# Performance work log

Measured on AMD Instinct MI355X. Metric: run time of the kernel, lower is better.

## Reference

```python
import jax, jax.numpy as jnp
import numpy as np


def _conv1d(x, w, b, pad):
    # x: (B, Cin, L), w: (Cout, Cin, K) -> (B, Cout, L)
    y = jax.lax.conv_general_dilated(x, w, window_strides=(1,), padding=[(pad, pad)],
                                     dimension_numbers=('NCH', 'OIH', 'NCH'))
    return y + b[None, :, None]


def setup_inputs() -> dict:
    V, E, H, D, K = 4096, 128, 256, 64, 512  # vocab, embed, hidden, code_dim, num_codes
    B, L = 16, 2048
    key = jax.random.key(0)
    ks = jax.random.split(key, 17)

    def g(k, shape, fan_in):
        return (jax.random.normal(k, shape, jnp.float32) / np.sqrt(fan_in)).astype(jnp.float32)

    x = jax.random.randint(ks[0], (B, L), 0, V)
    token_emb = (jax.random.normal(ks[1], (V, E), jnp.float32) * 0.02).at[0].set(0.0)  # pad_id=0
    # encoder convs: k3, k3, k1
    ew1 = g(ks[2], (H, E, 3), E * 3); eb1 = jnp.zeros((H,), jnp.float32)
    ew2 = g(ks[3], (H, H, 3), H * 3); eb2 = jnp.zeros((H,), jnp.float32)
    ew3 = g(ks[4], (D, H, 1), H);     eb3 = jnp.zeros((D,), jnp.float32)
    # VQ codebook: uniform(-1/K, 1/K)
    codebook = jax.random.uniform(ks[5], (K, D), jnp.float32, minval=-1.0 / K, maxval=1.0 / K)
    # decoder convs: k1, k3, k1
    dw1 = g(ks[6], (H, D, 1), D);     db1 = jnp.zeros((H,), jnp.float32)
    dw2 = g(ks[7], (H, H, 3), H * 3); db2 = jnp.zeros((H,), jnp.float32)
    dw3 = g(ks[8], (E, H, 1), H);     db3 = jnp.zeros((E,), jnp.float32)
    out_w = g(ks[9], (V, E), E);      out_b = jnp.zeros((V,), jnp.float32)
    return {"x": x, "token_emb": token_emb,
            "ew1": ew1, "eb1": eb1, "ew2": ew2, "eb2": eb2, "ew3": ew3, "eb3": eb3,
            "codebook": codebook,
            "dw1": dw1, "db1": db1, "dw2": dw2, "db2": db2, "dw3": dw3, "db3": db3,
            "out_w": out_w, "out_b": out_b}


def reference(x, token_emb, ew1, eb1, ew2, eb2, ew3, eb3, codebook,
              dw1, db1, dw2, db2, dw3, db3, out_w, out_b):
    B, L = x.shape
    emb = token_emb[x]                              # (B, L, E)
    h = jnp.transpose(emb, (0, 2, 1))               # (B, E, L)
    h = jax.nn.relu(_conv1d(h, ew1, eb1, 1))
    h = jax.nn.relu(_conv1d(h, ew2, eb2, 1))
    h = _conv1d(h, ew3, eb3, 0)
    z_e = jnp.transpose(h, (0, 2, 1))               # (B, L, D)
    D = z_e.shape[-1]
    # --- Vector quantization (eval mode: no EMA update) ---
    flat = z_e.reshape(-1, D)                       # (B*L, D)
    dists = (flat ** 2).sum(1, keepdims=True) - 2.0 * flat @ codebook.T + (codebook ** 2).sum(1)[None, :]
    codes = jnp.argmin(dists, axis=1)               # (B*L,)
    z_q = codebook[codes].reshape(B, L, D)
    z_q_st = z_e + jax.lax.stop_gradient(z_q - z_e)
    commit = jnp.mean((jax.lax.stop_gradient(z_e) - z_q) ** 2)
    loss_vq = 0.1 * commit                          # VQVAE passes commitment_cost=0.1
    # --- Decoder ---
    hd = jnp.transpose(z_q_st, (0, 2, 1))           # (B, D, L)
    hd = jax.nn.relu(_conv1d(hd, dw1, db1, 0))
    hd = jax.nn.relu(_conv1d(hd, dw2, db2, 1))
    hd = jax.nn.relu(_conv1d(hd, dw3, db3, 0))
    hd = jnp.transpose(hd, (0, 2, 1))               # (B, L, E)
    logits = hd @ out_w.T + out_b                   # (B, L, V)
    return logits, loss_vq, codes.reshape(B, L)
```

## Files before the change

### kernel.cpp

```cpp
#include <hip/hip_runtime.h>

constexpr int Bb = 16, Ll = 2048, Ee = 128, Hh = 256, Dd = 64, Kc = 512, Vv = 4096;
constexpr int NN = Bb * Ll;
constexpr int LOGITS = NN * Vv;

__global__ void transpose_w(const float* __restrict__ w, float* __restrict__ wt,
                            int Cout, int Cin, int KW) {
    int i = blockIdx.x * 256 + threadIdx.x;
    int total = Cout * Cin * KW;
    if (i >= total) return;
    int co  = i / (Cin * KW);
    int rem = i - co * (Cin * KW);
    int ci  = rem / KW;
    int k   = rem - ci * KW;
    wt[((size_t)(k * Cin + ci)) * Cout + co] = w[i];
}

__global__ void embed_kernel(const int* __restrict__ x,
                             const float4* __restrict__ te,
                             float4* __restrict__ out) {
    int gid = blockIdx.x * 256 + threadIdx.x;
    int n = gid >> 5;
    int c = gid & 31;
    out[gid] = te[((size_t)x[n] << 5) + c];
}

template <int KW, bool RELU, int BM, int BN, int TM, int TN>
__global__ __launch_bounds__(256) void gemm_conv(
    const float* __restrict__ A, const float* __restrict__ Wt,
    const float* __restrict__ bias, float* __restrict__ Y, int Cin, int Cout) {
    constexpr int BK = 16;
    const int tid = threadIdx.x;
    const int tx = tid % (BN / TN);
    const int ty = tid / (BN / TN);
    const int n0  = blockIdx.x * BM;
    const int co0 = blockIdx.y * BN;

    __shared__ float As[BK][BM + 4];
    __shared__ float Bs[BK][BN];

    float acc[TM][TN];
#pragma unroll
    for (int i = 0; i < TM; i++)
#pragma unroll
        for (int j = 0; j < TN; j++) acc[i][j] = 0.f;

    constexpr int A4 = BM * BK / (256 * 4);
    constexpr int B4 = BN * BK / (256 * 4);

    for (int k = 0; k < KW; ++k) {
        const int shift = k - (KW - 1) / 2;
        for (int ci0 = 0; ci0 < Cin; ci0 += BK) {
#pragma unroll
            for (int v = 0; v < A4; ++v) {
                int f4 = v * 256 + tid;
                int r  = f4 / (BK / 4);
                int c4 = f4 % (BK / 4);
                int n = n0 + r;
                float4 val = make_float4(0.f, 0.f, 0.f, 0.f);
                if (KW == 1) {
                    val = *(const float4*)(A + (size_t)n * Cin + ci0 + c4 * 4);
                } else {
                    int l  = n & (Ll - 1);
                    int sl = l + shift;
                    if ((unsigned)sl < (unsigned)Ll)
                        val = *(const float4*)(A + (size_t)(n + shift) * Cin + ci0 + c4 * 4);
                }
                As[c4 * 4 + 0][r] = val.x;
                As[c4 * 4 + 1][r] = val.y;
                As[c4 * 4 + 2][r] = val.z;
                As[c4 * 4 + 3][r] = val.w;
            }
#pragma unroll
            for (int v = 0; v < B4; ++v) {
                int f4 = v * 256 + tid;
                int c  = f4 / (BN / 4);
                int j4 = f4 % (BN / 4);
                float4 w4 = *(const float4*)(Wt + (size_t)(k * Cin + ci0 + c) * Cout + co0 + j4 * 4);
                *(float4*)(&Bs[c][j4 * 4]) = w4;
            }
            __syncthreads();
#pragma unroll
            for (int cc = 0; cc < BK; ++cc) {
                float a[TM], b[TN];
#pragma unroll
                for (int i = 0; i < TM; i += 4)
                    *(float4*)(&a[i]) = *(const float4*)(&As[cc][ty * TM + i]);
#pragma unroll
                for (int j = 0; j < TN; j += 4)
                    *(float4*)(&b[j]) = *(const float4*)(&Bs[cc][tx * TN + j]);
#pragma unroll
                for (int i = 0; i < TM; i++)
#pragma unroll
                    for (int j = 0; j < TN; j++)
                        acc[i][j] = fmaf(a[i], b[j], acc[i][j]);
            }
            __syncthreads();
        }
    }
#pragma unroll
    for (int i = 0; i < TM; i++) {
        int n = n0 + ty * TM + i;
#pragma unroll
        for (int j = 0; j < TN; j += 4) {
            int co = co0 + tx * TN + j;
            float4 r;
            r.x = acc[i][j + 0] + bias[co + 0];
            r.y = acc[i][j + 1] + bias[co + 1];
            r.z = acc[i][j + 2] + bias[co + 2];
            r.w = acc[i][j + 3] + bias[co + 3];
            if (RELU) {
                r.x = fmaxf(r.x, 0.f); r.y = fmaxf(r.y, 0.f);
                r.z = fmaxf(r.z, 0.f); r.w = fmaxf(r.w, 0.f);
            }
            *(float4*)(Y + (size_t)n * Cout + co) = r;
        }
    }
}

__global__ __launch_bounds__(256) void vq_kernel(
    const float* __restrict__ ze, const float* __restrict__ cb,
    int* __restrict__ codes_i, float* __restrict__ codes_f) {
    const int tid = threadIdx.x;
    const int tx = tid & 15, ty = tid >> 4;
    const int n0 = blockIdx.x * 64;

    __shared__ float Zs[Dd][64 + 4];
    __shared__ float Cs[Dd][64 + 4];
    __shared__ float bD[64][17];
    __shared__ int   bI[64][17];

#pragma unroll
    for (int v = 0; v < 4; ++v) {
        int f4 = v * 256 + tid;
        int row = f4 >> 4, d4 = f4 & 15;
        float4 z = *(const float4*)(ze + (size_t)(n0 + row) * Dd + d4 * 4);
        Zs[d4 * 4 + 0][row] = z.x;
        Zs[d4 * 4 + 1][row] = z.y;
        Zs[d4 * 4 + 2][row] = z.z;
        Zs[d4 * 4 + 3][row] = z.w;
    }

    float best[4];
    int   bidx[4];
#pragma unroll
    for (int i = 0; i < 4; i++) { best[i] = 3.4e38f; bidx[i] = 0; }

    for (int ch = 0; ch < Kc / 64; ++ch) {
        int c0 = ch * 64;
        __syncthreads();
#pragma unroll
        for (int v = 0; v < 4; ++v) {
            int f4 = v * 256 + tid;
            int j = f4 >> 4, d4 = f4 & 15;
            float4 w = *(const float4*)(cb + (size_t)(c0 + j) * Dd + d4 * 4);
            Cs[d4 * 4 + 0][j] = w.x;
            Cs[d4 * 4 + 1][j] = w.y;
            Cs[d4 * 4 + 2][j] = w.z;
            Cs[d4 * 4 + 3][j] = w.w;
        }
        __syncthreads();

        float dist[4][4];
#pragma unroll
        for (int i = 0; i < 4; i++)
#pragma unroll
            for (int j = 0; j < 4; j++) dist[i][j] = 0.f;

#pragma unroll 8
        for (int d = 0; d < Dd; ++d) {
            float a[4], b[4];
            *(float4*)a = *(const float4*)(&Zs[d][ty * 4]);
            *(float4*)b = *(const float4*)(&Cs[d][tx * 4]);
#pragma unroll
            for (int i = 0; i < 4; i++)
#pragma unroll
                for (int j = 0; j < 4; j++) {
                    float df = a[i] - b[j];
                    dist[i][j] = fmaf(df, df, dist[i][j]);
                }
        }
#pragma unroll
        for (int i = 0; i < 4; i++)
#pragma unroll
            for (int j = 0; j < 4; j++) {
                int ci = c0 + tx * 4 + j;
                if (dist[i][j] < best[i]) { best[i] = dist[i][j]; bidx[i] = ci; }
            }
    }
    __syncthreads();
#pragma unroll
    for (int i = 0; i < 4; i++) {
        bD[ty * 4 + i][tx] = best[i];
        bI[ty * 4 + i][tx] = bidx[i];
    }
    __syncthreads();
    if (tid < 64) {
        float bd = bD[tid][0];
        int   bi = bI[tid][0];
        for (int t = 1; t < 16; ++t) {
            float d = bD[tid][t];
            int   ix = bI[tid][t];
            if (d < bd || (d == bd && ix < bi)) { bd = d; bi = ix; }
        }
        codes_i[n0 + tid] = bi;
        codes_f[n0 + tid] = (float)bi;
    }
}

__global__ void gather_zq(const int* __restrict__ codes,
                          const float4* __restrict__ cb, float4* __restrict__ zq) {
    int gid = blockIdx.x * 256 + threadIdx.x;
    int n = gid >> 4, c = gid & 15;
    zq[gid] = cb[((size_t)codes[n] << 4) + c];
}

__global__ __launch_bounds__(256) void commit_partial(
    const float* __restrict__ ze, const float* __restrict__ zq,
    float* __restrict__ partial) {
    float s = 0.f;
    for (int i = blockIdx.x * 256 + threadIdx.x; i < NN * Dd; i += 1024 * 256) {
        float d = ze[i] - zq[i];
        s = fmaf(d, d, s);
    }
    for (int off = 32; off; off >>= 1) s += __shfl_down(s, off, 64);
    __shared__ float w[4];
    int lane = threadIdx.x & 63, wv = threadIdx.x >> 6;
    if (lane == 0) w[wv] = s;
    __syncthreads();
    if (threadIdx.x == 0) partial[blockIdx.x] = w[0] + w[1] + w[2] + w[3];
}

__global__ void commit_final(const float* __restrict__ partial, float* __restrict__ loss) {
    float s = 0.f;
    for (int i = threadIdx.x; i < 1024; i += 256) s += partial[i];
    for (int off = 32; off; off >>= 1) s += __shfl_down(s, off, 64);
    __shared__ float w[4];
    int lane = threadIdx.x & 63, wv = threadIdx.x >> 6;
    if (lane == 0) w[wv] = s;
    __syncthreads();
    if (threadIdx.x == 0)
        loss[0] = 0.1f * (w[0] + w[1] + w[2] + w[3]) / (float)(NN * Dd);
}

extern "C" void kernel_launch(void* const* d_in, const int* in_sizes, int n_in,
                              void* d_out, int out_size, void* d_ws, size_t ws_size,
                              hipStream_t stream) {
    const int*   x    = (const int*)d_in[0];
    const float* te   = (const float*)d_in[1];
    const float* ew1  = (const float*)d_in[2];
    const float* eb1  = (const float*)d_in[3];
    const float* ew2  = (const float*)d_in[4];
    const float* eb2  = (const float*)d_in[5];
    const float* ew3  = (const float*)d_in[6];
    const float* eb3  = (const float*)d_in[7];
    const float* cb   = (const float*)d_in[8];
    const float* dw1  = (const float*)d_in[9];
    const float* db1  = (const float*)d_in[10];
    const float* dw2  = (const float*)d_in[11];
    const float* db2  = (const float*)d_in[12];
    const float* dw3  = (const float*)d_in[13];
    const float* db3  = (const float*)d_in[14];
    const float* outw = (const float*)d_in[15];
    const float* outb = (const float*)d_in[16];

    char* ws = (char*)d_ws;
    size_t off = 0;
    auto alloc = [&](size_t bytes) -> void* {
        void* p = ws + off;
        off = (off + bytes + 255) & ~(size_t)255;
        return p;
    };
    float* bufA   = (float*)alloc((size_t)NN * Ee * 4);
    float* bufB   = (float*)alloc((size_t)NN * Hh * 4);
    float* bufC   = (float*)alloc((size_t)NN * Hh * 4);
    float* bufZ   = (float*)alloc((size_t)NN * Dd * 4);
    float* bufQ   = (float*)alloc((size_t)NN * Dd * 4);
    int*   codesi = (int*)alloc((size_t)NN * 4);
    float* part   = (float*)alloc(1024 * 4);
    float* wt_e1  = (float*)alloc((size_t)3 * Ee * Hh * 4);
    float* wt_e2  = (float*)alloc((size_t)3 * Hh * Hh * 4);
    float* wt_e3  = (float*)alloc((size_t)Hh * Dd * 4);
    float* wt_d1  = (float*)alloc((size_t)Dd * Hh * 4);
    float* wt_d2  = (float*)alloc((size_t)3 * Hh * Hh * 4);
    float* wt_d3  = (float*)alloc((size_t)Hh * Ee * 4);
    float* wt_o   = (float*)alloc((size_t)Ee * Vv * 4);

    float* out       = (float*)d_out;
    float* out_loss  = out + (size_t)LOGITS;
    float* out_codes = out_loss + 1;

    auto tg = [](int n) { return dim3((n + 255) / 256); };
    transpose_w<<<tg(Hh * Ee * 3), 256, 0, stream>>>(ew1, wt_e1, Hh, Ee, 3);
    transpose_w<<<tg(Hh * Hh * 3), 256, 0, stream>>>(ew2, wt_e2, Hh, Hh, 3);
    transpose_w<<<tg(Dd * Hh),     256, 0, stream>>>(ew3, wt_e3, Dd, Hh, 1);
    transpose_w<<<tg(Hh * Dd),     256, 0, stream>>>(dw1, wt_d1, Hh, Dd, 1);
    transpose_w<<<tg(Hh * Hh * 3), 256, 0, stream>>>(dw2, wt_d2, Hh, Hh, 3);
    transpose_w<<<tg(Ee * Hh),     256, 0, stream>>>(dw3, wt_d3, Ee, Hh, 1);
    transpose_w<<<tg(Vv * Ee),     256, 0, stream>>>(outw, wt_o, Vv, Ee, 1);

    embed_kernel<<<dim3(NN * 32 / 256), 256, 0, stream>>>(x, (const float4*)te, (float4*)bufA);

    gemm_conv<3, true, 128, 128, 8, 8><<<dim3(NN / 128, Hh / 128), 256, 0, stream>>>(bufA, wt_e1, eb1, bufB, Ee, Hh);
    gemm_conv<3, true, 128, 128, 8, 8><<<dim3(NN / 128, Hh / 128), 256, 0, stream>>>(bufB, wt_e2, eb2, bufC, Hh, Hh);
    gemm_conv<1, false, 64, 64, 4, 4><<<dim3(NN / 64, 1), 256, 0, stream>>>(bufC, wt_e3, eb3, bufZ, Hh, Dd);

    vq_kernel<<<dim3(NN / 64), 256, 0, stream>>>(bufZ, cb, codesi, out_codes);
    gather_zq<<<dim3(NN * 16 / 256), 256, 0, stream>>>(codesi, (const float4*)cb, (float4*)bufQ);
    commit_partial<<<dim3(1024), 256, 0, stream>>>(bufZ, bufQ, part);
    commit_final<<<dim3(1), 256, 0, stream>>>(part, out_loss);

    gemm_conv<1, true, 128, 128, 8, 8><<<dim3(NN / 128, Hh / 128), 256, 0, stream>>>(bufQ, wt_d1, db1, bufB, Dd, Hh);
    gemm_conv<3, true, 128, 128, 8, 8><<<dim3(NN / 128, Hh / 128), 256, 0, stream>>>(bufB, wt_d2, db2, bufC, Hh, Hh);
    gemm_conv<1, true, 128, 128, 8, 8><<<dim3(NN / 128, Ee / 128), 256, 0, stream>>>(bufC, wt_d3, db3, bufA, Hh, Ee);

    gemm_conv<1, false, 128, 128, 8, 8><<<dim3(NN / 128, Vv / 128), 256, 0, stream>>>(bufA, wt_o, outb, out, Ee, Vv);
}
```

Measured before the change: 1.413 ms.

## Compute output projection with bf16x3 split MFMA GEMM

Replaces the FP32 SIMT GEMM for the final vocab projection with a bf16 MFMA kernel. Each FP32 operand is split into hi and lo bf16 parts and laid out along an extended K dimension of 3*E, so one MFMA GEMM accumulates hi*hi + hi*lo + lo*hi and approximates FP32 accuracy. Operand tiles are loaded with direct global-to-LDS loads. This adds an activation split pass plus extra bf16 buffers, and its accuracy is below true FP32 because the lo*lo term is dropped.

```diff
diff --git a/kernel.cpp b/kernel.cpp
--- a/kernel.cpp
+++ b/kernel.cpp
@@ -3,6 +3,9 @@
 constexpr int Bb = 16, Ll = 2048, Ee = 128, Hh = 256, Dd = 64, Kc = 512, Vv = 4096;
 constexpr int NN = Bb * Ll;
 constexpr int LOGITS = NN * Vv;
+
+typedef __attribute__((ext_vector_type(8))) short bf16x8;
+typedef __attribute__((ext_vector_type(4))) float f32x4;
 
 __global__ void transpose_w(const float* __restrict__ w, float* __restrict__ wt,
                             int Cout, int Cin, int KW) {
@@ -23,6 +26,117 @@
     int n = gid >> 5;
     int c = gid & 31;
     out[gid] = te[((size_t)x[n] << 5) + c];
+}
+
+__device__ __forceinline__ unsigned short f2bf_rne(float f) {
+    unsigned int u = __float_as_uint(f);
+    unsigned int r = (u + 0x7fffu + ((u >> 16) & 1u)) >> 16;
+    return (unsigned short)r;
+}
+__device__ __forceinline__ float bf2f(unsigned short h) {
+    return __uint_as_float((unsigned int)h << 16);
+}
+
+template <bool LO_MID>
+__global__ void split3(const float* __restrict__ in, short* __restrict__ out, int K) {
+    int idx = blockIdx.x * 256 + threadIdx.x;
+    int m = idx / K;
+    int k = idx - m * K;
+    float a = in[idx];
+    unsigned short hi = f2bf_rne(a);
+    unsigned short lo = f2bf_rne(a - bf2f(hi));
+    size_t base = (size_t)m * (3 * K) + k;
+    out[base]         = (short)hi;
+    out[base + K]     = (short)(LO_MID ? lo : hi);
+    out[base + 2 * K] = (short)(LO_MID ? hi : lo);
+}
+
+__device__ __forceinline__ void gload16(const void* g, void* l) {
+    __builtin_amdgcn_global_load_lds(
+        (const __attribute__((address_space(1))) unsigned int*)g,
+        (__attribute__((address_space(3))) unsigned int*)l, 16, 0, 0);
+}
+
+template <bool RELU>
+__global__ __launch_bounds__(256) void gemm_mfma(
+    const short* __restrict__ A3, const short* __restrict__ B3,
+    const float* __restrict__ bias, float* __restrict__ Y,
+    int KK, int Nout) {
+    __shared__ short As[4096];
+    __shared__ short Bs[4096];
+
+    const int tid  = threadIdx.x;
+    const int lane = tid & 63;
+    const int wid  = tid >> 6;
+    const int ntile = Nout >> 7;
+    const int tm = blockIdx.x / ntile;
+    const int tn = blockIdx.x - tm * ntile;
+    const int m0 = tm << 7;
+    const int n0 = tn << 7;
+
+    const int wm = wid >> 1, wn = wid & 1;
+    const int lr = lane & 15;
+    const int kg = lane >> 4;
+
+    f32x4 acc[4][4];
+#pragma unroll
+    for (int i = 0; i < 4; ++i)
+#pragma unroll
+        for (int j = 0; j < 4; ++j)
+#pragma unroll
+            for (int q = 0; q < 4; ++q) acc[i][j][q] = 0.f;
+
+    const short* Ag = A3 + (size_t)m0 * KK;
+    const short* Bg = B3 + (size_t)n0 * KK;
+
+    for (int k0 = 0; k0 < KK; k0 += 32) {
+#pragma unroll
+        for (int j = 0; j < 2; ++j) {
+            const short* g = Ag + (size_t)(j * 64 + lane) * KK + k0 + wid * 8;
+            short* l = As + (size_t)(wid * 128 + j * 64) * 8;
+            gload16(g, l);
+        }
+#pragma unroll
+        for (int j = 0; j < 2; ++j) {
+            const short* g = Bg + (size_t)(j * 64 + lane) * KK + k0 + wid * 8;
+            short* l = Bs + (size_t)(wid * 128 + j * 64) * 8;
+            gload16(g, l);
+        }
+        __syncthreads();
+
+        bf16x8 af[4], bfr[4];
+#pragma unroll
+        for (int i = 0; i < 4; ++i)
+            af[i] = *reinterpret_cast<const bf16x8*>(
+                &As[(size_t)(kg * 128 + wm * 64 + i * 16 + lr) * 8]);
+#pragma unroll
+        for (int j = 0; j < 4; ++j)
+            bfr[j] = *reinterpret_cast<const bf16x8*>(
+                &Bs[(size_t)(kg * 128 + wn * 64 + j * 16 + lr) * 8]);
+#pragma unroll
+        for (int i = 0; i < 4; ++i)
+#pragma unroll
+            for (int j = 0; j < 4; ++j)
+                acc[i][j] = __builtin_amdgcn_mfma_f32_16x16x32_bf16(
+                    af[i], bfr[j], acc[i][j], 0, 0, 0);
+        __syncthreads();
+    }
+
+#pragma unroll
+    for (int i = 0; i < 4; ++i) {
+        int r0 = m0 + wm * 64 + i * 16 + kg * 4;
+#pragma unroll
+        for (int j = 0; j < 4; ++j) {
+            int col = n0 + wn * 64 + j * 16 + lr;
+            float bv = bias[col];
+#pragma unroll
+            for (int q = 0; q < 4; ++q) {
+                float v = acc[i][j][q] + bv;
+                if (RELU) v = fmaxf(v, 0.f);
+                Y[(size_t)(r0 + q) * Nout + col] = v;
+            }
+        }
+    }
 }
 
 template <int KW, bool RELU, int BM, int BN, int TM, int TN>
@@ -284,7 +398,8 @@
     float* wt_d1  = (float*)alloc((size_t)Dd * Hh * 4);
     float* wt_d2  = (float*)alloc((size_t)3 * Hh * Hh * 4);
     float* wt_d3  = (float*)alloc((size_t)Hh * Ee * 4);
-    float* wt_o   = (float*)alloc((size_t)Ee * Vv * 4);
+    short* a3     = (short*)alloc((size_t)NN * 3 * Ee * 2);
+    short* w3     = (short*)alloc((size_t)Vv * 3 * Ee * 2);
 
     float* out       = (float*)d_out;
     float* out_loss  = out + (size_t)LOGITS;
@@ -297,7 +412,7 @@
     transpose_w<<<tg(Hh * Dd),     256, 0, stream>>>(dw1, wt_d1, Hh, Dd, 1);
     transpose_w<<<tg(Hh * Hh * 3), 256, 0, stream>>>(dw2, wt_d2, Hh, Hh, 3);
     transpose_w<<<tg(Ee * Hh),     256, 0, stream>>>(dw3, wt_d3, Ee, Hh, 1);
-    transpose_w<<<tg(Vv * Ee),     256, 0, stream>>>(outw, wt_o, Vv, Ee, 1);
+    split3<false><<<tg(Vv * Ee), 256, 0, stream>>>(outw, w3, Ee);
 
     embed_kernel<<<dim3(NN * 32 / 256), 256, 0, stream>>>(x, (const float4*)te, (float4*)bufA);
 
@@ -314,5 +429,7 @@
     gemm_conv<3, true, 128, 128, 8, 8><<<dim3(NN / 128, Hh / 128), 256, 0, stream>>>(bufB, wt_d2, db2, bufC, Hh, Hh);
     gemm_conv<1, true, 128, 128, 8, 8><<<dim3(NN / 128, Ee / 128), 256, 0, stream>>>(bufC, wt_d3, db3, bufA, Hh, Ee);
 
-    gemm_conv<1, false, 128, 128, 8, 8><<<dim3(NN / 128, Vv / 128), 256, 0, stream>>>(bufA, wt_o, outb, out, Ee, Vv);
-}
+    split3<true><<<tg(NN * Ee), 256, 0, stream>>>(bufA, a3, Ee);
+    gemm_mfma<false><<<dim3((NN / 128) * (Vv / 128)), 256, 0, stream>>>(
+        a3, w3, outb, out, 3 * Ee, Vv);
+}
```

New measurement: 1.292 ms. -8.5%, faster.
